# Kernel optimization log

Measured on AMD Instinct MI355X. Metric: run time of the kernel, lower is better.

The kernel has to match this reference:

```python
import jax, jax.numpy as jnp
import numpy as np

B, T, C = 2, 2048, 1024
H, D = 16, 64
SCALE = D ** -0.5


def setup_inputs() -> dict:
    key = jax.random.key(0)
    k1, k2, k3 = jax.random.split(key, 3)
    hidden_states = jax.random.normal(k1, (B, T, C), dtype=jnp.float32)
    # rotary tables: standard RoPE angles, shape (T, D//2)
    inv_freq = 1.0 / (10000.0 ** (np.arange(0, D, 2, dtype=np.float32) / D))
    ang = np.arange(T, dtype=np.float32)[:, None] * inv_freq[None, :]
    cos = jnp.asarray(np.cos(ang))
    sin = jnp.asarray(np.sin(ang))
    qkv_w = jax.random.normal(k2, (3 * H * D, C), dtype=jnp.float32) * 0.02
    qkv_b = jnp.zeros((3 * H * D,), dtype=jnp.float32)
    proj_w = jax.random.normal(k3, (C, H * D), dtype=jnp.float32) * 0.02
    proj_b = jnp.zeros((C,), dtype=jnp.float32)
    return dict(hidden_states=hidden_states, cos=cos, sin=sin,
                qkv_w=qkv_w, qkv_b=qkv_b, proj_w=proj_w, proj_b=proj_b)


def _rotary(x, cos, sin):
    # x: (B, H, T, D); cos/sin: (T, D//2) broadcast over batch and heads
    c = cos[None, None, :, :]
    s = sin[None, None, :, :]
    x1, x2 = x[..., ::2], x[..., 1::2]
    return jnp.concatenate([x1 * c - x2 * s, x1 * s + x2 * c], axis=-1)


def reference(hidden_states, cos, sin, qkv_w, qkv_b, proj_w, proj_b):
    b, t, c = hidden_states.shape
    qkv = hidden_states @ qkv_w.T + qkv_b          # (B, T, 3*H*D)
    q, k, v = jnp.split(qkv, 3, axis=-1)
    # (B, T, H, D) -> (B, H, T, D)
    q = q.reshape(b, t, H, D).transpose(0, 2, 1, 3)
    k = k.reshape(b, t, H, D).transpose(0, 2, 1, 3)
    v = v.reshape(b, t, H, D).transpose(0, 2, 1, 3)
    q = _rotary(q, cos, sin)
    k = _rotary(k, cos, sin)
    scores = jnp.einsum('bhqd,bhkd->bhqk', q, k) * SCALE
    # causal mask: -inf above the diagonal
    mask = jnp.triu(jnp.full((t, t), -jnp.inf, dtype=scores.dtype), k=1)
    scores = scores + mask[None, None, :, :]
    attn = jax.nn.softmax(scores, axis=-1)
    out = jnp.einsum('bhqk,bhkd->bhqd', attn, v)   # (B, H, T, D)
    out = out.transpose(0, 2, 1, 3).reshape(b, t, c)
    return out @ proj_w.T + proj_b
```

## Files before the change

### kernel.cpp

```cpp
#include <hip/hip_runtime.h>
#include <stdint.h>

#define B_ 2
#define T_ 2048
#define C_ 1024
#define H_ 16
#define D_ 64
#define SCALE_L2E 0.1803368801111244f

typedef unsigned short ushort_t;
typedef __attribute__((ext_vector_type(8))) __bf16 bf16x8;
typedef __attribute__((ext_vector_type(4))) float f32x4;
typedef __attribute__((ext_vector_type(4))) unsigned short ushort4_t;

__device__ __forceinline__ float bf2f(ushort_t u) {
    union { unsigned int u; float f; } v; v.u = ((unsigned int)u) << 16; return v.f;
}
__device__ __forceinline__ ushort_t f2bf(float f) {
    union { __bf16 h; ushort_t u; } v; v.h = (__bf16)f; return v.u;
}

__device__ __forceinline__ void gl16(const void* g, void* l) {
    __builtin_amdgcn_global_load_lds(
        (const __attribute__((address_space(1))) void*)g,
        (__attribute__((address_space(3))) void*)l, 16, 0, 0);
}

__device__ __forceinline__ f32x4 mfma16(bf16x8 a, bf16x8 b, f32x4 c) {
    return __builtin_amdgcn_mfma_f32_16x16x32_bf16(a, b, c, 0, 0, 0);
}

__global__ __launch_bounds__(256) void cvt3_kernel(const float* __restrict__ a, ushort_t* __restrict__ oa, int na,
                                                   const float* __restrict__ b, ushort_t* __restrict__ ob, int nb,
                                                   const float* __restrict__ c, ushort_t* __restrict__ oc, int nc) {
    int total4 = (na + nb + nc) >> 2;
    int stride = gridDim.x * blockDim.x;
    for (int i = blockIdx.x * blockDim.x + threadIdx.x; i < total4; i += stride) {
        int e = i << 2;
        const float* src; ushort_t* dst; int off;
        if (e < na) { src = a; dst = oa; off = e; }
        else if (e < na + nb) { src = b; dst = ob; off = e - na; }
        else { src = c; dst = oc; off = e - na - nb; }
        float4 v = *(const float4*)(src + off);
        ushort4_t o;
        o.x = f2bf(v.x); o.y = f2bf(v.y); o.z = f2bf(v.z); o.w = f2bf(v.w);
        *(ushort4_t*)(dst + off) = o;
    }
}

__global__ __launch_bounds__(256) void gemm_proj(const ushort_t* __restrict__ A,
                                                 const ushort_t* __restrict__ Bw,
                                                 const float* __restrict__ bias,
                                                 float* __restrict__ outf,
                                                 int M, int N, int K, int nxt) {
    int q = gridDim.x >> 3;
    int nid = (blockIdx.x & 7) * q + (blockIdx.x >> 3);
    int bx = nid % nxt, by = nid / nxt;

    __shared__ ushort_t sm[16384];
    int tid = threadIdx.x, w = tid >> 6, lane = tid & 63;
    int lr = lane >> 4, lc = lane & 15;
    int wr = w >> 1, wc = w & 1;
    int row0 = by * 128, col0 = bx * 128;

    f32x4 acc[4][4];
#pragma unroll
    for (int mf = 0; mf < 4; ++mf)
#pragma unroll
        for (int nf = 0; nf < 4; ++nf) acc[mf][nf] = (f32x4){0.f, 0.f, 0.f, 0.f};

    auto stageg = [&](int buf, int k0) {
#pragma unroll
        for (int j = 0; j < 2; ++j) {
            int idx = j * 256 + tid;
            int r = idx >> 2, c = (idx & 3) * 8;
            gl16(A + (size_t)(row0 + r) * K + k0 + c, &sm[buf * 8192 + idx * 8]);
            gl16(Bw + (size_t)(col0 + r) * K + k0 + c, &sm[buf * 8192 + 4096 + idx * 8]);
        }
    };

    stageg(0, 0);
    asm volatile("s_waitcnt vmcnt(0)" ::: "memory");
    __builtin_amdgcn_s_barrier();

    for (int k0 = 0; k0 < K; k0 += 32) {
        int cur = (k0 >> 5) & 1;
        if (k0 + 32 < K) stageg(cur ^ 1, k0 + 32);
        const ushort_t* As = &sm[cur * 8192];
        const ushort_t* Bs = &sm[cur * 8192 + 4096];
        bf16x8 af[4], bfr[4];
#pragma unroll
        for (int mf = 0; mf < 4; ++mf)
            af[mf] = *(const bf16x8*)&As[(wr * 64 + mf * 16 + lc) * 32 + 8 * lr];
#pragma unroll
        for (int nf = 0; nf < 4; ++nf)
            bfr[nf] = *(const bf16x8*)&Bs[(wc * 64 + nf * 16 + lc) * 32 + 8 * lr];
        __builtin_amdgcn_s_setprio(1);
#pragma unroll
        for (int mf = 0; mf < 4; ++mf)
#pragma unroll
            for (int nf = 0; nf < 4; ++nf)
                acc[mf][nf] = mfma16(af[mf], bfr[nf], acc[mf][nf]);
        __builtin_amdgcn_s_setprio(0);
        asm volatile("s_waitcnt vmcnt(0)" ::: "memory");
        __builtin_amdgcn_s_barrier();
    }
#pragma unroll
    for (int mf = 0; mf < 4; ++mf)
#pragma unroll
        for (int nf = 0; nf < 4; ++nf) {
            int col = col0 + wc * 64 + nf * 16 + lc;
            float bv = bias[col];
#pragma unroll
            for (int r = 0; r < 4; ++r) {
                int row = row0 + wr * 64 + mf * 16 + 4 * lr + r;
                outf[(size_t)row * N + col] = acc[mf][nf][r] + bv;
            }
        }
}

__global__ __launch_bounds__(256) void gemm_qkv_rope(const ushort_t* __restrict__ A,
                                                     const ushort_t* __restrict__ Bw,
                                                     const float* __restrict__ bias,
                                                     const float* __restrict__ cosT,
                                                     const float* __restrict__ sinT,
                                                     ushort_t* __restrict__ Qr,
                                                     ushort_t* __restrict__ Kr,
                                                     ushort_t* __restrict__ Vt) {
    const int K = 1024;
    int nid = (blockIdx.x & 7) * 96 + (blockIdx.x >> 3);
    int bx = nid % 24, by = nid / 24;

    __shared__ ushort_t sm[16384];
    int tid = threadIdx.x, w = tid >> 6, lane = tid & 63;
    int lr = lane >> 4, lc = lane & 15;
    int wr = w >> 1, wc = w & 1;
    int row0 = by * 128, col0 = bx * 128;

    f32x4 acc[4][4];
#pragma unroll
    for (int mf = 0; mf < 4; ++mf)
#pragma unroll
        for (int nf = 0; nf < 4; ++nf) acc[mf][nf] = (f32x4){0.f, 0.f, 0.f, 0.f};

    auto stageg = [&](int buf, int k0) {
#pragma unroll
        for (int j = 0; j < 2; ++j) {
            int idx = j * 256 + tid;
            int r = idx >> 2, c = (idx & 3) * 8;
            gl16(A + (size_t)(row0 + r) * K + k0 + c, &sm[buf * 8192 + idx * 8]);
            gl16(Bw + (size_t)(col0 + r) * K + k0 + c, &sm[buf * 8192 + 4096 + idx * 8]);
        }
    };

    stageg(0, 0);
    asm volatile("s_waitcnt vmcnt(0)" ::: "memory");
    __builtin_amdgcn_s_barrier();

    for (int k0 = 0; k0 < K; k0 += 32) {
        int cur = (k0 >> 5) & 1;
        if (k0 + 32 < K) stageg(cur ^ 1, k0 + 32);
        const ushort_t* As = &sm[cur * 8192];
        const ushort_t* Bs = &sm[cur * 8192 + 4096];
        bf16x8 af[4], bfr[4];
#pragma unroll
        for (int mf = 0; mf < 4; ++mf)
            af[mf] = *(const bf16x8*)&As[(wr * 64 + mf * 16 + lc) * 32 + 8 * lr];
#pragma unroll
        for (int nf = 0; nf < 4; ++nf)
            bfr[nf] = *(const bf16x8*)&Bs[(wc * 64 + nf * 16 + lc) * 32 + 8 * lr];
        __builtin_amdgcn_s_setprio(1);
#pragma unroll
        for (int mf = 0; mf < 4; ++mf)
#pragma unroll
            for (int nf = 0; nf < 4; ++nf)
                acc[mf][nf] = mfma16(af[mf], bfr[nf], acc[mf][nf]);
        __builtin_amdgcn_s_setprio(0);
        asm volatile("s_waitcnt vmcnt(0)" ::: "memory");
        __builtin_amdgcn_s_barrier();
    }

    if (bx < 16) {
        const int typ = bx >> 3;
        ushort_t* dstb = typ ? Kr : Qr;
#pragma unroll
        for (int nf = 0; nf < 4; ++nf) {
            int fullc = col0 + wc * 64 + nf * 16 + lc;
            int gc = fullc & 1023;
            int h = gc >> 6;
            int d2 = (gc & 63) >> 1;
            int odd = gc & 1;
            float bv = bias[fullc];
#pragma unroll
            for (int mf = 0; mf < 4; ++mf)
#pragma unroll
                for (int r = 0; r < 4; ++r) {
                    int row = row0 + wr * 64 + mf * 16 + 4 * lr + r;
                    int bb = row >> 11, t = row & 2047;
                    float v = acc[mf][nf][r] + bv;
                    float pv = __shfl_xor(v, 1, 64);
                    float cth = cosT[t * 32 + d2], sth = sinT[t * 32 + d2];
                    float o = odd ? (pv * sth + v * cth) : (v * cth - pv * sth);
                    if (typ == 0) o *= SCALE_L2E;
                    int od = odd ? (d2 + 32) : d2;
                    dstb[((size_t)(bb * H_ + h) * T_ + t) * D_ + od] = f2bf(o);
                }
        }
    } else {
        int bb = row0 >> 11;
        int tb = row0 & 2047;
#pragma unroll 1
        for (int half = 0; half < 2; ++half) {
            __syncthreads();
            if (wc == half) {
#pragma unroll
                for (int nf = 0; nf < 4; ++nf) {
                    int fullc = col0 + wc * 64 + nf * 16 + lc;
                    float bv = bias[fullc];
                    int c = nf * 16 + lc;
#pragma unroll
                    for (int mf = 0; mf < 4; ++mf)
#pragma unroll
                        for (int r = 0; r < 4; ++r) {
                            int tl = wr * 64 + mf * 16 + 4 * lr + r;
                            sm[c * 136 + tl] = f2bf(acc[mf][nf][r] + bv);
                        }
                }
            }
            __syncthreads();
            int h = ((bx - 16) << 1) + half;
#pragma unroll
            for (int it = 0; it < 8; ++it) {
                int idx = it * 256 + tid;
                int c = idx >> 5, j = idx & 31;
                ushort4_t vv = *(const ushort4_t*)&sm[c * 136 + 4 * j];
                *(ushort4_t*)&Vt[((size_t)(bb * H_ + h) * D_ + c) * T_ + tb + 4 * j] = vv;
            }
        }
    }
}

__global__ __launch_bounds__(256) void attn_kernel(const ushort_t* __restrict__ Qr,
                                                   const ushort_t* __restrict__ Kr,
                                                   const ushort_t* __restrict__ Vt,
                                                   ushort_t* __restrict__ attnb) {
    int id = blockIdx.x;
    int x = id & 7;
    int c = (id >> 3) & 31;
    int g = id >> 8;
    int bh = x + 8 * g;
    int qt;
    if (g == 0) qt = c;
    else if (g == 1) qt = 31 - c;
    else if (g == 2) qt = (c + 16) & 31;
    else qt = 31 - ((c + 16) & 31);
    int b = bh >> 4, h = bh & 15;

    const ushort_t* Qp = Qr + (size_t)bh * T_ * D_;
    const ushort_t* Kp = Kr + (size_t)bh * T_ * D_;
    const ushort_t* Vp = Vt + (size_t)bh * D_ * T_;
    int tid = threadIdx.x, w = tid >> 6, lane = tid & 63;
    int lr = lane >> 4, lc = lane & 15;

    __shared__ ushort_t Ks[2][64 * 64];
    __shared__ ushort_t Vs[2][64 * 64];
    __shared__ ushort_t Ps[4][16 * 64];

    bf16x8 ones;
#pragma unroll
    for (int i = 0; i < 8; ++i) ones[i] = (__bf16)1.0f;

    auto stage = [&](int buf, int kt) {
        int t0 = kt * 64;
#pragma unroll
        for (int j = 0; j < 2; ++j) {
            int idx = j * 256 + tid;
            int row = idx >> 3, ch = idx & 7;
            int sch = ch ^ (row & 7);
            gl16(Kp + (size_t)(t0 + row) * D_ + sch * 8, &Ks[buf][idx * 8]);
            gl16(Vp + (size_t)row * T_ + t0 + sch * 8, &Vs[buf][idx * 8]);
        }
    };

    int qrow = qt * 64 + w * 16 + lc;
    bf16x8 qf0 = *(const bf16x8*)(Qp + (size_t)qrow * D_ + 8 * lr);
    bf16x8 qf1 = *(const bf16x8*)(Qp + (size_t)qrow * D_ + 32 + 8 * lr);

    float m_s = 0.f;
    f32x4 acc[4], acc_l;
#pragma unroll
    for (int f = 0; f < 4; ++f) acc[f] = (f32x4){0.f, 0.f, 0.f, 0.f};
    acc_l = (f32x4){0.f, 0.f, 0.f, 0.f};

    stage(0, 0);
    asm volatile("s_waitcnt vmcnt(0)" ::: "memory");
    __builtin_amdgcn_s_barrier();

    for (int kt = 0; kt <= qt; ++kt) {
        int cur = kt & 1;
        if (kt < qt) stage(cur ^ 1, kt + 1);
        int t0 = kt * 64;

        f32x4 sv[4];
        __builtin_amdgcn_s_setprio(1);
#pragma unroll
        for (int f = 0; f < 4; ++f) {
            sv[f] = (f32x4){-m_s, -m_s, -m_s, -m_s};
            int row = 16 * f + lc;
#pragma unroll
            for (int kk = 0; kk < 2; ++kk) {
                bf16x8 kf = *(const bf16x8*)&Ks[cur][row * 64 + (((lr + 4 * kk) ^ (row & 7)) * 8)];
                sv[f] = mfma16(kf, kk ? qf1 : qf0, sv[f]);
            }
        }
        __builtin_amdgcn_s_setprio(0);

        float lm = -1e30f;
        if (kt == qt) {
#pragma unroll
            for (int f = 0; f < 4; ++f)
#pragma unroll
                for (int r = 0; r < 4; ++r) {
                    int kg = t0 + 16 * f + 4 * lr + r;
                    float v = sv[f][r];
                    v = (kg > qrow) ? -1e30f : v;
                    sv[f][r] = v;
                    lm = fmaxf(lm, v);
                }
        } else {
#pragma unroll
            for (int f = 0; f < 4; ++f)
#pragma unroll
                for (int r = 0; r < 4; ++r)
                    lm = fmaxf(lm, sv[f][r]);
        }

        if (!__all(lm <= 8.0f)) {
            float tm = fmaxf(lm, __shfl_xor(lm, 16, 64));
            tm = fmaxf(tm, __shfl_xor(tm, 32, 64));
            float d = fmaxf(tm, 0.f);
            m_s += d;
            float alpha = exp2f(-d);
            float ar[4];
#pragma unroll
            for (int r = 0; r < 4; ++r) ar[r] = __shfl(alpha, 4 * lr + r, 64);
#pragma unroll
            for (int r = 0; r < 4; ++r) {
                acc_l[r] *= ar[r];
#pragma unroll
                for (int f = 0; f < 4; ++f) acc[f][r] *= ar[f == 0 ? r : r];
            }
#pragma unroll
            for (int f = 0; f < 4; ++f)
#pragma unroll
                for (int r = 0; r < 4; ++r) sv[f][r] -= d;
        }

#pragma unroll
        for (int f = 0; f < 4; ++f) {
            ushort4_t pk;
            pk.x = f2bf(exp2f(sv[f][0]));
            pk.y = f2bf(exp2f(sv[f][1]));
            pk.z = f2bf(exp2f(sv[f][2]));
            pk.w = f2bf(exp2f(sv[f][3]));
            *(ushort4_t*)&Ps[w][lc * 64 + (((4 * f + lr) ^ (lc & 14)) << 2)] = pk;
        }

        __builtin_amdgcn_s_setprio(1);
#pragma unroll
        for (int kk = 0; kk < 2; ++kk) {
            bf16x8 pf = *(const bf16x8*)&Ps[w][lc * 64 + (((8 * kk + 2 * lr) ^ (lc & 14)) << 2)];
            acc_l = mfma16(pf, ones, acc_l);
#pragma unroll
            for (int f = 0; f < 4; ++f) {
                int vrow = 16 * f + lc;
                bf16x8 vfr = *(const bf16x8*)&Vs[cur][vrow * 64 + (((lr + 4 * kk) ^ (vrow & 7)) * 8)];
                acc[f] = mfma16(pf, vfr, acc[f]);
            }
        }
        __builtin_amdgcn_s_setprio(0);

        asm volatile("s_waitcnt vmcnt(0)" ::: "memory");
        __builtin_amdgcn_s_barrier();
    }

    float inv[4];
#pragma unroll
    for (int r = 0; r < 4; ++r) inv[r] = 1.f / acc_l[r];
#pragma unroll
    for (int f = 0; f < 4; ++f)
#pragma unroll
        for (int r = 0; r < 4; ++r) {
            int t = qt * 64 + w * 16 + 4 * lr + r;
            attnb[((size_t)(b * T_ + t)) * 1024 + h * 64 + 16 * f + lc] =
                f2bf(acc[f][r] * inv[r]);
        }
}

extern "C" void kernel_launch(void* const* d_in, const int* in_sizes, int n_in,
                              void* d_out, int out_size, void* d_ws, size_t ws_size,
                              hipStream_t stream) {
    const float* hs     = (const float*)d_in[0];
    const float* cosp   = (const float*)d_in[1];
    const float* sinp   = (const float*)d_in[2];
    const float* qkv_w  = (const float*)d_in[3];
    const float* qkv_b  = (const float*)d_in[4];
    const float* proj_w = (const float*)d_in[5];
    const float* proj_b = (const float*)d_in[6];
    float* out = (float*)d_out;

    const int M = B_ * T_;
    ushort_t* Xb     = (ushort_t*)d_ws;
    ushort_t* Wqkvb  = Xb + (size_t)M * C_;
    ushort_t* Wprojb = Wqkvb + (size_t)3072 * C_;
    ushort_t* Qr     = Wprojb + (size_t)C_ * C_;
    ushort_t* Kr     = Qr + (size_t)B_ * H_ * T_ * D_;
    ushort_t* Vt     = Kr + (size_t)B_ * H_ * T_ * D_;
    ushort_t* attnb  = Vt + (size_t)B_ * H_ * T_ * D_;

    cvt3_kernel<<<2048, 256, 0, stream>>>(hs, Xb, M * C_,
                                          qkv_w, Wqkvb, 3072 * C_,
                                          proj_w, Wprojb, C_ * C_);

    gemm_qkv_rope<<<768, 256, 0, stream>>>(Xb, Wqkvb, qkv_b, cosp, sinp, Qr, Kr, Vt);

    attn_kernel<<<1024, 256, 0, stream>>>(Qr, Kr, Vt, attnb);

    gemm_proj<<<256, 256, 0, stream>>>(attnb, Wprojb, proj_b, out, M, C_, C_, 1024 / 128);
}
```

Measured before the change: 129.1 us.

## Schedule attention tiles dynamically via atomic work queue, longest-first, single-buffered V

The attention kernel becomes persistent: each block repeatedly takes a work item from a global atomic counter. Items are ordered so that the longest causal query tiles are handed out first, which is meant to reduce tail imbalance across compute units. V is now single-buffered and staged at the top of each key step, with a partial vmcnt wait before the PV stage, which frees LDS. The cost is an extra memset launch to reset the counter, plus an atomic and a block barrier per work item.

```diff
diff --git a/kernel.cpp b/kernel.cpp
--- a/kernel.cpp
+++ b/kernel.cpp
@@ -243,158 +243,173 @@
 __global__ __launch_bounds__(256) void attn_kernel(const ushort_t* __restrict__ Qr,
                                                    const ushort_t* __restrict__ Kr,
                                                    const ushort_t* __restrict__ Vt,
-                                                   ushort_t* __restrict__ attnb) {
-    int id = blockIdx.x;
-    int x = id & 7;
-    int c = (id >> 3) & 31;
-    int g = id >> 8;
-    int bh = x + 8 * g;
-    int qt;
-    if (g == 0) qt = c;
-    else if (g == 1) qt = 31 - c;
-    else if (g == 2) qt = (c + 16) & 31;
-    else qt = 31 - ((c + 16) & 31);
-    int b = bh >> 4, h = bh & 15;
-
-    const ushort_t* Qp = Qr + (size_t)bh * T_ * D_;
-    const ushort_t* Kp = Kr + (size_t)bh * T_ * D_;
-    const ushort_t* Vp = Vt + (size_t)bh * D_ * T_;
+                                                   ushort_t* __restrict__ attnb,
+                                                   unsigned int* __restrict__ cnt) {
     int tid = threadIdx.x, w = tid >> 6, lane = tid & 63;
     int lr = lane >> 4, lc = lane & 15;
 
     __shared__ ushort_t Ks[2][64 * 64];
-    __shared__ ushort_t Vs[2][64 * 64];
+    __shared__ ushort_t Vs[64 * 64];
     __shared__ ushort_t Ps[4][16 * 64];
+    volatile int* itemp = (volatile int*)&Ps[0][0];
 
     bf16x8 ones;
 #pragma unroll
     for (int i = 0; i < 8; ++i) ones[i] = (__bf16)1.0f;
 
-    auto stage = [&](int buf, int kt) {
-        int t0 = kt * 64;
-#pragma unroll
-        for (int j = 0; j < 2; ++j) {
-            int idx = j * 256 + tid;
-            int row = idx >> 3, ch = idx & 7;
-            int sch = ch ^ (row & 7);
-            gl16(Kp + (size_t)(t0 + row) * D_ + sch * 8, &Ks[buf][idx * 8]);
-            gl16(Vp + (size_t)row * T_ + t0 + sch * 8, &Vs[buf][idx * 8]);
-        }
-    };
-
-    int qrow = qt * 64 + w * 16 + lc;
-    bf16x8 qf0 = *(const bf16x8*)(Qp + (size_t)qrow * D_ + 8 * lr);
-    bf16x8 qf1 = *(const bf16x8*)(Qp + (size_t)qrow * D_ + 32 + 8 * lr);
-
-    float m_s = 0.f;
-    f32x4 acc[4], acc_l;
-#pragma unroll
-    for (int f = 0; f < 4; ++f) acc[f] = (f32x4){0.f, 0.f, 0.f, 0.f};
-    acc_l = (f32x4){0.f, 0.f, 0.f, 0.f};
-
-    stage(0, 0);
-    asm volatile("s_waitcnt vmcnt(0)" ::: "memory");
-    __builtin_amdgcn_s_barrier();
-
-    for (int kt = 0; kt <= qt; ++kt) {
-        int cur = kt & 1;
-        if (kt < qt) stage(cur ^ 1, kt + 1);
-        int t0 = kt * 64;
-
-        f32x4 sv[4];
-        __builtin_amdgcn_s_setprio(1);
-#pragma unroll
-        for (int f = 0; f < 4; ++f) {
-            sv[f] = (f32x4){-m_s, -m_s, -m_s, -m_s};
-            int row = 16 * f + lc;
+    for (;;) {
+        if (tid == 0) *itemp = (int)atomicAdd(cnt, 1u);
+        __syncthreads();
+        int t = *itemp;
+        if (t >= 1024) break;
+        int qt = 31 - (t >> 5);
+        int bh = t & 31;
+        int b = bh >> 4, h = bh & 15;
+
+        const ushort_t* Qp = Qr + (size_t)bh * T_ * D_;
+        const ushort_t* Kp = Kr + (size_t)bh * T_ * D_;
+        const ushort_t* Vp = Vt + (size_t)bh * D_ * T_;
+
+        auto stageK = [&](int buf, int kt) {
+            int t0 = kt * 64;
+#pragma unroll
+            for (int j = 0; j < 2; ++j) {
+                int idx = j * 256 + tid;
+                int row = idx >> 3, ch = idx & 7;
+                int sch = ch ^ (row & 7);
+                gl16(Kp + (size_t)(t0 + row) * D_ + sch * 8, &Ks[buf][idx * 8]);
+            }
+        };
+        auto stageV = [&](int kt) {
+            int t0 = kt * 64;
+#pragma unroll
+            for (int j = 0; j < 2; ++j) {
+                int idx = j * 256 + tid;
+                int row = idx >> 3, ch = idx & 7;
+                int sch = ch ^ (row & 7);
+                gl16(Vp + (size_t)row * T_ + t0 + sch * 8, &Vs[idx * 8]);
+            }
+        };
+
+        int qrow = qt * 64 + w * 16 + lc;
+        bf16x8 qf0 = *(const bf16x8*)(Qp + (size_t)qrow * D_ + 8 * lr);
+        bf16x8 qf1 = *(const bf16x8*)(Qp + (size_t)qrow * D_ + 32 + 8 * lr);
+
+        float m_s = 0.f;
+        f32x4 acc[4], acc_l;
+#pragma unroll
+        for (int f = 0; f < 4; ++f) acc[f] = (f32x4){0.f, 0.f, 0.f, 0.f};
+        acc_l = (f32x4){0.f, 0.f, 0.f, 0.f};
+
+        stageK(0, 0);
+
+        for (int kt = 0; kt <= qt; ++kt) {
+            int cur = kt & 1;
+            int t0 = kt * 64;
+            asm volatile("s_waitcnt vmcnt(0)" ::: "memory");
+            __builtin_amdgcn_s_barrier();
+            stageV(kt);
+            if (kt < qt) stageK(cur ^ 1, kt + 1);
+
+            f32x4 sv[4];
+            __builtin_amdgcn_s_setprio(1);
+#pragma unroll
+            for (int f = 0; f < 4; ++f) {
+                sv[f] = (f32x4){-m_s, -m_s, -m_s, -m_s};
+                int row = 16 * f + lc;
+#pragma unroll
+                for (int kk = 0; kk < 2; ++kk) {
+                    bf16x8 kf = *(const bf16x8*)&Ks[cur][row * 64 + (((lr + 4 * kk) ^ (row & 7)) * 8)];
+                    sv[f] = mfma16(kf, kk ? qf1 : qf0, sv[f]);
+                }
+            }
+            __builtin_amdgcn_s_setprio(0);
+
+            float lm = -1e30f;
+            if (kt == qt) {
+#pragma unroll
+                for (int f = 0; f < 4; ++f)
+#pragma unroll
+                    for (int r = 0; r < 4; ++r) {
+                        int kg = t0 + 16 * f + 4 * lr + r;
+                        float v = sv[f][r];
+                        v = (kg > qrow) ? -1e30f : v;
+                        sv[f][r] = v;
+                        lm = fmaxf(lm, v);
+                    }
+            } else {
+#pragma unroll
+                for (int f = 0; f < 4; ++f)
+#pragma unroll
+                    for (int r = 0; r < 4; ++r)
+                        lm = fmaxf(lm, sv[f][r]);
+            }
+
+            if (!__all(lm <= 8.0f)) {
+                float tm = fmaxf(lm, __shfl_xor(lm, 16, 64));
+                tm = fmaxf(tm, __shfl_xor(tm, 32, 64));
+                float d = fmaxf(tm, 0.f);
+                m_s += d;
+                float alpha = exp2f(-d);
+                float ar[4];
+#pragma unroll
+                for (int r = 0; r < 4; ++r) ar[r] = __shfl(alpha, 4 * lr + r, 64);
+#pragma unroll
+                for (int r = 0; r < 4; ++r) {
+                    acc_l[r] *= ar[r];
+#pragma unroll
+                    for (int f = 0; f < 4; ++f) acc[f][r] *= ar[r];
+                }
+#pragma unroll
+                for (int f = 0; f < 4; ++f)
+#pragma unroll
+                    for (int r = 0; r < 4; ++r) sv[f][r] -= d;
+            }
+
+#pragma unroll
+            for (int f = 0; f < 4; ++f) {
+                ushort4_t pk;
+                pk.x = f2bf(exp2f(sv[f][0]));
+                pk.y = f2bf(exp2f(sv[f][1]));
+                pk.z = f2bf(exp2f(sv[f][2]));
+                pk.w = f2bf(exp2f(sv[f][3]));
+                *(ushort4_t*)&Ps[w][lc * 64 + (((4 * f + lr) ^ (lc & 14)) << 2)] = pk;
+            }
+
+            if (kt < qt) {
+                asm volatile("s_waitcnt vmcnt(2)" ::: "memory");
+            } else {
+                asm volatile("s_waitcnt vmcnt(0)" ::: "memory");
+            }
+            __builtin_amdgcn_s_barrier();
+
+            __builtin_amdgcn_s_setprio(1);
 #pragma unroll
             for (int kk = 0; kk < 2; ++kk) {
-                bf16x8 kf = *(const bf16x8*)&Ks[cur][row * 64 + (((lr + 4 * kk) ^ (row & 7)) * 8)];
-                sv[f] = mfma16(kf, kk ? qf1 : qf0, sv[f]);
-            }
-        }
-        __builtin_amdgcn_s_setprio(0);
-
-        float lm = -1e30f;
-        if (kt == qt) {
-#pragma unroll
-            for (int f = 0; f < 4; ++f)
-#pragma unroll
-                for (int r = 0; r < 4; ++r) {
-                    int kg = t0 + 16 * f + 4 * lr + r;
-                    float v = sv[f][r];
-                    v = (kg > qrow) ? -1e30f : v;
-                    sv[f][r] = v;
-                    lm = fmaxf(lm, v);
+                bf16x8 pf = *(const bf16x8*)&Ps[w][lc * 64 + (((8 * kk + 2 * lr) ^ (lc & 14)) << 2)];
+                acc_l = mfma16(pf, ones, acc_l);
+#pragma unroll
+                for (int f = 0; f < 4; ++f) {
+                    int vrow = 16 * f + lc;
+                    bf16x8 vfr = *(const bf16x8*)&Vs[vrow * 64 + (((lr + 4 * kk) ^ (vrow & 7)) * 8)];
+                    acc[f] = mfma16(pf, vfr, acc[f]);
                 }
-        } else {
-#pragma unroll
-            for (int f = 0; f < 4; ++f)
-#pragma unroll
-                for (int r = 0; r < 4; ++r)
-                    lm = fmaxf(lm, sv[f][r]);
-        }
-
-        if (!__all(lm <= 8.0f)) {
-            float tm = fmaxf(lm, __shfl_xor(lm, 16, 64));
-            tm = fmaxf(tm, __shfl_xor(tm, 32, 64));
-            float d = fmaxf(tm, 0.f);
-            m_s += d;
-            float alpha = exp2f(-d);
-            float ar[4];
-#pragma unroll
-            for (int r = 0; r < 4; ++r) ar[r] = __shfl(alpha, 4 * lr + r, 64);
+            }
+            __builtin_amdgcn_s_setprio(0);
+        }
+
+        float inv[4];
+#pragma unroll
+        for (int r = 0; r < 4; ++r) inv[r] = 1.f / acc_l[r];
+#pragma unroll
+        for (int f = 0; f < 4; ++f)
 #pragma unroll
             for (int r = 0; r < 4; ++r) {
-                acc_l[r] *= ar[r];
-#pragma unroll
-                for (int f = 0; f < 4; ++f) acc[f][r] *= ar[f == 0 ? r : r];
-            }
-#pragma unroll
-            for (int f = 0; f < 4; ++f)
-#pragma unroll
-                for (int r = 0; r < 4; ++r) sv[f][r] -= d;
-        }
-
-#pragma unroll
-        for (int f = 0; f < 4; ++f) {
-            ushort4_t pk;
-            pk.x = f2bf(exp2f(sv[f][0]));
-            pk.y = f2bf(exp2f(sv[f][1]));
-            pk.z = f2bf(exp2f(sv[f][2]));
-            pk.w = f2bf(exp2f(sv[f][3]));
-            *(ushort4_t*)&Ps[w][lc * 64 + (((4 * f + lr) ^ (lc & 14)) << 2)] = pk;
-        }
-
-        __builtin_amdgcn_s_setprio(1);
-#pragma unroll
-        for (int kk = 0; kk < 2; ++kk) {
-            bf16x8 pf = *(const bf16x8*)&Ps[w][lc * 64 + (((8 * kk + 2 * lr) ^ (lc & 14)) << 2)];
-            acc_l = mfma16(pf, ones, acc_l);
-#pragma unroll
-            for (int f = 0; f < 4; ++f) {
-                int vrow = 16 * f + lc;
-                bf16x8 vfr = *(const bf16x8*)&Vs[cur][vrow * 64 + (((lr + 4 * kk) ^ (vrow & 7)) * 8)];
-                acc[f] = mfma16(pf, vfr, acc[f]);
-            }
-        }
-        __builtin_amdgcn_s_setprio(0);
-
-        asm volatile("s_waitcnt vmcnt(0)" ::: "memory");
-        __builtin_amdgcn_s_barrier();
+                int tq = qt * 64 + w * 16 + 4 * lr + r;
+                attnb[((size_t)(b * T_ + tq)) * 1024 + h * 64 + 16 * f + lc] =
+                    f2bf(acc[f][r] * inv[r]);
+            }
     }
-
-    float inv[4];
-#pragma unroll
-    for (int r = 0; r < 4; ++r) inv[r] = 1.f / acc_l[r];
-#pragma unroll
-    for (int f = 0; f < 4; ++f)
-#pragma unroll
-        for (int r = 0; r < 4; ++r) {
-            int t = qt * 64 + w * 16 + 4 * lr + r;
-            attnb[((size_t)(b * T_ + t)) * 1024 + h * 64 + 16 * f + lc] =
-                f2bf(acc[f][r] * inv[r]);
-        }
 }
 
 extern "C" void kernel_launch(void* const* d_in, const int* in_sizes, int n_in,
@@ -417,6 +432,7 @@
     ushort_t* Kr     = Qr + (size_t)B_ * H_ * T_ * D_;
     ushort_t* Vt     = Kr + (size_t)B_ * H_ * T_ * D_;
     ushort_t* attnb  = Vt + (size_t)B_ * H_ * T_ * D_;
+    unsigned int* cnt = (unsigned int*)(attnb + (size_t)M * C_);
 
     cvt3_kernel<<<2048, 256, 0, stream>>>(hs, Xb, M * C_,
                                           qkv_w, Wqkvb, 3072 * C_,
@@ -424,7 +440,9 @@
 
     gemm_qkv_rope<<<768, 256, 0, stream>>>(Xb, Wqkvb, qkv_b, cosp, sinp, Qr, Kr, Vt);
 
-    attn_kernel<<<1024, 256, 0, stream>>>(Qr, Kr, Vt, attnb);
+    hipMemsetAsync((void*)cnt, 0, 4, stream);
+
+    attn_kernel<<<1280, 256, 0, stream>>>(Qr, Kr, Vt, attnb, cnt);
 
     gemm_proj<<<256, 256, 0, stream>>>(attnb, Wprojb, proj_b, out, M, C_, C_, 1024 / 128);
 }
```

Result: slower. 139.7 us (+8.2%).
